# Optimization experiments

Measured on AMD Instinct MI355X. Metric: run time of the kernel, lower is better.

Reference implementation:

```python
import jax, jax.numpy as jnp
import numpy as np

B, NKV, NQ, D, H = 4, 2048, 1024, 1024, 16
HD = D // H


def setup_inputs() -> dict:
    key = jax.random.key(0)
    ks = jax.random.split(key, 9)
    s = 0.02
    return {
        "x": jax.random.normal(ks[0], (B, NKV, D), jnp.float32),
        "y": jax.random.normal(ks[1], (B, NQ, D), jnp.float32),
        "mask": jax.random.randint(ks[2], (B, NQ, NKV), 0, 2, jnp.int32),
        "W_kv": jax.random.normal(ks[3], (D, 2 * D), jnp.float32) * s,
        "b_kv": jnp.zeros((2 * D,), jnp.float32),
        "W_q": jax.random.normal(ks[4], (D, D), jnp.float32) * s,
        "b_q": jnp.zeros((D,), jnp.float32),
        "W_o": jax.random.normal(ks[5], (D, D), jnp.float32) * s,
        "b_o": jnp.zeros((D,), jnp.float32),
    }


def reference(x, y, mask, W_kv, b_kv, W_q, b_q, W_o, b_o):
    b, nkv, _ = x.shape
    nq = y.shape[1]
    kv = x @ W_kv + b_kv                                  # [B, NKV, 2D]
    q = y @ W_q + b_q                                     # [B, NQ, D]
    kv = kv.reshape(b, nkv, H, 2 * HD).transpose(0, 2, 1, 3)  # [B,H,NKV,2HD]
    q = q.reshape(b, nq, H, HD).transpose(0, 2, 1, 3)         # [B,H,NQ,HD]
    k, v = kv[..., :HD], kv[..., HD:]
    scores = jnp.einsum('bhqd,bhkd->bhqk', q, k) / jnp.sqrt(jnp.float32(HD))
    scores = jnp.where(mask[:, None, :, :] == 0, jnp.float32(-1e20), scores)
    attn = jax.nn.softmax(scores, axis=-1)
    vals = jnp.einsum('bhqk,bhkd->bhqd', attn, v)          # [B,H,NQ,HD]
    vals = vals.transpose(0, 2, 1, 3).reshape(b, nq, D)
    return vals @ W_o + b_o
```

## Files before the change

### kernel.cpp

```cpp
#include <hip/hip_runtime.h>
#include <hip/hip_bf16.h>
#include <math.h>

#define B_   4
#define NKV_ 2048
#define NQ_  1024
#define D_   1024
#define H_   16
#define HD_  64

typedef __attribute__((ext_vector_type(8))) short bf16x8;
typedef __attribute__((ext_vector_type(4))) float f32x4;

#define MFMA16x32(a, b, c) __builtin_amdgcn_mfma_f32_16x16x32_bf16((a), (b), (c), 0, 0, 0)

#define SC_LOG2 0.1803368801111244f

__device__ __forceinline__ short f2bf(float f) {
    unsigned u = __builtin_bit_cast(unsigned, f);
    u = (u + 0x7fff + ((u >> 16) & 1)) >> 16;
    return (short)u;
}
__device__ __forceinline__ unsigned cvt_pk_bf16(float lo, float hi) {
    unsigned r;
    asm("v_cvt_pk_bf16_f32 %0, %1, %2" : "=v"(r) : "v"(lo), "v"(hi));
    return r;
}
__device__ __forceinline__ void gload_lds16(const void* g, void* l) {
    __builtin_amdgcn_global_load_lds(
        (const __attribute__((address_space(1))) void*)g,
        (__attribute__((address_space(3))) void*)l, 16, 0, 0);
}
__device__ __forceinline__ void barrier_raw() {
    asm volatile("" ::: "memory");
    __builtin_amdgcn_s_barrier();
    asm volatile("" ::: "memory");
}

__global__ __launch_bounds__(256)
void prep(const float* __restrict__ Wkv, short* __restrict__ Tkv,
          const float* __restrict__ Wq,  short* __restrict__ Tq,
          const float* __restrict__ Wo,  short* __restrict__ To,
          const int* __restrict__ mask,  unsigned short* __restrict__ m16,
          const float* __restrict__ x,   short* __restrict__ xh, int n4x,
          const float* __restrict__ y,   short* __restrict__ yh, int n4y)
{
    const int bid = (int)blockIdx.x;
    if (bid < 4096) {
        const float* W; short* T; int K, N, bx, by;
        if (bid < 2048)      { W = Wkv; T = Tkv; K = D_; N = 2 * D_; bx = bid & 63;          by = bid >> 6; }
        else if (bid < 3072) { W = Wq;  T = Tq;  K = D_; N = D_;     bx = (bid - 2048) & 31; by = (bid - 2048) >> 5; }
        else                 { W = Wo;  T = To;  K = D_; N = D_;     bx = (bid - 3072) & 31; by = (bid - 3072) >> 5; }
        __shared__ float tile[32][33];
        const int tx = threadIdx.x & 31, ty = threadIdx.x >> 5;
        const int n0 = bx * 32, k0 = by * 32;
#pragma unroll
        for (int i = 0; i < 4; ++i)
            tile[ty + 8 * i][tx] = W[(size_t)(k0 + ty + 8 * i) * N + n0 + tx];
        __syncthreads();
#pragma unroll
        for (int i = 0; i < 4; ++i)
            T[(size_t)(n0 + ty + 8 * i) * K + k0 + tx] = f2bf(tile[tx][ty + 8 * i]);
    } else if (bid < 4608) {
        const int w = (bid - 4096) * 256 + threadIdx.x;
        const int4* pp = reinterpret_cast<const int4*>(mask + (size_t)w * 64);
        unsigned wg0 = 0, wg1 = 0, wg2 = 0, wg3 = 0;
#pragma unroll
        for (int i = 0; i < 16; ++i) {
            const int4 v = pp[i];
            const unsigned nib = (unsigned)(v.x != 0) | ((unsigned)(v.y != 0) << 1)
                               | ((unsigned)(v.z != 0) << 2) | ((unsigned)(v.w != 0) << 3);
            const unsigned sh = 4u * (unsigned)(i >> 2);
            if ((i & 3) == 0) wg0 |= nib << sh;
            else if ((i & 3) == 1) wg1 |= nib << sh;
            else if ((i & 3) == 2) wg2 |= nib << sh;
            else wg3 |= nib << sh;
        }
        ushort4 o;
        o.x = (unsigned short)wg0; o.y = (unsigned short)wg1;
        o.z = (unsigned short)wg2; o.w = (unsigned short)wg3;
        reinterpret_cast<ushort4*>(m16)[w] = o;
    } else {
        const int ntot = n4x + n4y;
        for (int i = (bid - 4608) * 256 + threadIdx.x; i < ntot; i += 2048 * 256) {
            const float4 v = (i < n4x)
                ? reinterpret_cast<const float4*>(x)[i]
                : reinterpret_cast<const float4*>(y)[i - n4x];
            short4 h;
            h.x = f2bf(v.x); h.y = f2bf(v.y); h.z = f2bf(v.z); h.w = f2bf(v.w);
            if (i < n4x) reinterpret_cast<short4*>(xh)[i] = h;
            else         reinterpret_cast<short4*>(yh)[i - n4x] = h;
        }
    }
}

__device__ __forceinline__
void gemm_body(int mode, int bidl,
               const short* __restrict__ Ahi, const short* __restrict__ Bhi,
               const float* __restrict__ bias, void* __restrict__ out0,
               void* __restrict__ out1, int M, int N, int K)
{
    __shared__ short At[3][4096];
    __shared__ short Bt[3][4096];

    const int t    = threadIdx.x;
    const int wave = t >> 6;
    const int lane = t & 63;
    const int fr   = lane & 15;
    const int kq   = lane >> 4;

    const int gx  = N >> 7;
    const int gy  = M >> 7;
    const int lgx = __builtin_ctz(gx);
    const int xcd = bidl & 7;
    const int j   = bidl >> 3;
    const int m0  = (xcd * (gy >> 3) + (j >> lgx)) * 128;
    const int n0  = (j & (gx - 1)) * 128;

    const int wm0 = (wave & 1) * 64;
    const int wn0 = (wave >> 1) * 64;
    const int NT  = K >> 5;

    const int r1 = t >> 2,         g1 = (t & 3) ^ ((r1 >> 1) & 3);
    const int r2 = (t + 256) >> 2, g2 = (t & 3) ^ ((r2 >> 1) & 3);

    f32x4 acc[4][4];
#pragma unroll
    for (int i = 0; i < 4; ++i)
#pragma unroll
        for (int j2 = 0; j2 < 4; ++j2) acc[i][j2] = f32x4{0.f, 0.f, 0.f, 0.f};

    auto stage = [&](int sb, int it) {
        const int kk = it << 5;
        gload_lds16(Ahi + (size_t)(m0 + r1) * K + kk + 8 * g1, &At[sb][wave * 512]);
        gload_lds16(Ahi + (size_t)(m0 + r2) * K + kk + 8 * g2, &At[sb][2048 + wave * 512]);
        gload_lds16(Bhi + (size_t)(n0 + r1) * K + kk + 8 * g1, &Bt[sb][wave * 512]);
        gload_lds16(Bhi + (size_t)(n0 + r2) * K + kk + 8 * g2, &Bt[sb][2048 + wave * 512]);
    };

    stage(0, 0);
    if (NT > 1) stage(1, 1);

    const int gsw = ((kq ^ ((fr >> 1) & 3)) << 3);
    for (int it = 0; it < NT; ++it) {
        if (it + 1 < NT) asm volatile("s_waitcnt vmcnt(4)" ::: "memory");
        else             asm volatile("s_waitcnt vmcnt(0)" ::: "memory");
        barrier_raw();

        const int cb = it % 3;
        bf16x8 af[4], bf[4];
#pragma unroll
        for (int i = 0; i < 4; ++i) {
            af[i] = *reinterpret_cast<const bf16x8*>(&At[cb][(wm0 + i * 16 + fr) * 32 + gsw]);
            bf[i] = *reinterpret_cast<const bf16x8*>(&Bt[cb][(wn0 + i * 16 + fr) * 32 + gsw]);
        }
        if (it + 2 < NT) stage((it + 2) % 3, it + 2);

        __builtin_amdgcn_s_setprio(1);
#pragma unroll
        for (int i = 0; i < 4; ++i)
#pragma unroll
            for (int j2 = 0; j2 < 4; ++j2)
                acc[i][j2] = MFMA16x32(af[i], bf[j2], acc[i][j2]);
        __builtin_amdgcn_s_setprio(0);
    }

#pragma unroll
    for (int i = 0; i < 4; ++i) {
#pragma unroll
        for (int j2 = 0; j2 < 4; ++j2) {
#pragma unroll
            for (int r = 0; r < 4; ++r) {
                const int m = m0 + wm0 + i * 16 + (lane >> 4) * 4 + r;
                const int n = n0 + wn0 + j2 * 16 + fr;
                const float v = acc[i][j2][r] + bias[n];
                if (mode == 0) {
                    short* K_ = (short*)out0;
                    short* Vt = (short*)out1;
                    const int b  = m >> 11;
                    const int nk = m & 2047;
                    const int h  = n >> 7;
                    const int c  = n & 127;
                    const int bh = b * H_ + h;
                    if (c < 64)
                        K_[(((size_t)bh * NKV_ + nk) << 6) + c] = f2bf(v);
                    else
                        Vt[((size_t)bh * 64 + (c - 64)) * NKV_ + nk] = f2bf(v);
                } else if (mode == 1) {
                    short* Q_ = (short*)out0;
                    const int b = m >> 10;
                    const int q = m & 1023;
                    const int h = n >> 6;
                    const int d = n & 63;
                    Q_[(((size_t)(b * H_ + h) * NQ_ + q) << 6) + d] =
                        f2bf(v * SC_LOG2);
                } else {
                    ((float*)out0)[(size_t)m * N + n] = v;
                }
            }
        }
    }
}

__global__ __launch_bounds__(256)
void proj(const short* __restrict__ xhi, const short* __restrict__ Wkvt,
          const float* __restrict__ b_kv, short* __restrict__ Kbf,
          short* __restrict__ Vtbf,
          const short* __restrict__ yhi, const short* __restrict__ Wqt,
          const float* __restrict__ b_q, short* __restrict__ Qbf)
{
    const int bid = (int)blockIdx.x;
    if (bid < 1024)
        gemm_body(0, bid, xhi, Wkvt, b_kv, Kbf, Vtbf, B_ * NKV_, 2 * D_, D_);
    else
        gemm_body(1, bid - 1024, yhi, Wqt, b_q, Qbf, nullptr, B_ * NQ_, D_, D_);
}

__global__ __launch_bounds__(256)
void ogemm(const short* __restrict__ Ahi, const short* __restrict__ Bhi,
           const float* __restrict__ bias, float* __restrict__ out)
{
    __shared__ short At[3][2048];
    __shared__ short Bt[3][4096];

    const int M = B_ * NQ_, N = D_, K = D_;
    const int t    = threadIdx.x;
    const int wave = t >> 6;
    const int lane = t & 63;
    const int fr   = lane & 15;
    const int kq   = lane >> 4;

    const int gx  = N >> 7;
    const int gy  = M >> 6;
    const int lgx = __builtin_ctz(gx);
    const int bid = (int)blockIdx.x;
    const int xcd = bid & 7;
    const int j   = bid >> 3;
    const int m0  = (xcd * (gy >> 3) + (j >> lgx)) * 64;
    const int n0  = (j & (gx - 1)) * 128;

    const int wm0 = (wave & 1) * 32;
    const int wn0 = (wave >> 1) * 64;
    const int NT  = K >> 5;

    const int rA = t >> 2, gA = (t & 3) ^ ((rA >> 1) & 3);
    const int r1 = t >> 2,         g1 = (t & 3) ^ ((r1 >> 1) & 3);
    const int r2 = (t + 256) >> 2, g2 = (t & 3) ^ ((r2 >> 1) & 3);

    f32x4 acc[2][4];
#pragma unroll
    for (int i = 0; i < 2; ++i)
#pragma unroll
        for (int j2 = 0; j2 < 4; ++j2) acc[i][j2] = f32x4{0.f, 0.f, 0.f, 0.f};

    auto stage = [&](int sb, int it) {
        const int kk = it << 5;
        gload_lds16(Ahi + (size_t)(m0 + rA) * K + kk + 8 * gA, &At[sb][wave * 512]);
        gload_lds16(Bhi + (size_t)(n0 + r1) * K + kk + 8 * g1, &Bt[sb][wave * 512]);
        gload_lds16(Bhi + (size_t)(n0 + r2) * K + kk + 8 * g2, &Bt[sb][2048 + wave * 512]);
    };

    stage(0, 0);
    if (NT > 1) stage(1, 1);

    const int gsw = ((kq ^ ((fr >> 1) & 3)) << 3);
    for (int it = 0; it < NT; ++it) {
        if (it + 1 < NT) asm volatile("s_waitcnt vmcnt(3)" ::: "memory");
        else             asm volatile("s_waitcnt vmcnt(0)" ::: "memory");
        barrier_raw();

        const int cb = it % 3;
        bf16x8 af[2], bf[4];
#pragma unroll
        for (int i = 0; i < 2; ++i)
            af[i] = *reinterpret_cast<const bf16x8*>(&At[cb][(wm0 + i * 16 + fr) * 32 + gsw]);
#pragma unroll
        for (int i = 0; i < 4; ++i)
            bf[i] = *reinterpret_cast<const bf16x8*>(&Bt[cb][(wn0 + i * 16 + fr) * 32 + gsw]);
        if (it + 2 < NT) stage((it + 2) % 3, it + 2);

        __builtin_amdgcn_s_setprio(1);
#pragma unroll
        for (int i = 0; i < 2; ++i)
#pragma unroll
            for (int j2 = 0; j2 < 4; ++j2)
                acc[i][j2] = MFMA16x32(af[i], bf[j2], acc[i][j2]);
        __builtin_amdgcn_s_setprio(0);
    }

#pragma unroll
    for (int i = 0; i < 2; ++i)
#pragma unroll
        for (int j2 = 0; j2 < 4; ++j2)
#pragma unroll
            for (int r = 0; r < 4; ++r) {
                const int m = m0 + wm0 + i * 16 + (lane >> 4) * 4 + r;
                const int n = n0 + wn0 + j2 * 16 + fr;
                out[(size_t)m * N + n] = acc[i][j2][r] + bias[n];
            }
}

__global__ __launch_bounds__(512)
void attn_mfma(const short* __restrict__ Q, const short* __restrict__ K,
               const short* __restrict__ Vt,
               const unsigned short* __restrict__ m16,
               float* __restrict__ Opart, float* __restrict__ Lpart)
{
    __shared__ short KtL[2][4096];
    __shared__ short VtL[2][4096];
    __shared__ short PsL[8192];

    const int t    = threadIdx.x;
    const int wave = t >> 6;
    const int lane = t & 63;
    const int fr   = lane & 15;
    const int g    = lane >> 4;

    const int bid  = (int)blockIdx.x;
    const int xcd  = bid & 7;
    const int j    = bid >> 3;
    const int bh   = xcd * 8 + (j >> 4);
    const int rest = j & 15;
    const int half = rest & 1;
    const int b    = bh >> 4;
    const int h    = bh & 15;
    const int wq0  = (rest >> 1) * 128 + wave * 16;

    const int kts = half * 16;
    const int kte = kts + 16;

    const short* Kg  = K  + (size_t)bh * NKV_ * 64;
    const short* Vtg = Vt + (size_t)bh * 64 * NKV_;

    bf16x8 qf0, qf1;
    {
        const short* Qg = Q + ((size_t)bh * NQ_ + wq0 + fr) * 64 + g * 8;
        qf0 = *reinterpret_cast<const bf16x8*>(Qg);
        qf1 = *reinterpret_cast<const bf16x8*>(Qg + 32);
    }

    bf16x8 ones;
#pragma unroll
    for (int i = 0; i < 8; ++i) ones[i] = (short)0x3F80;

    f32x4 acc_o[4];
#pragma unroll
    for (int n = 0; n < 4; ++n) acc_o[n] = f32x4{0.f, 0.f, 0.f, 0.f};
    f32x4 lacc = f32x4{0.f, 0.f, 0.f, 0.f};

    const unsigned short* mbp =
        m16 + ((size_t)b * NQ_ + wq0 + fr) * (NKV_ / 64) * 4 + g;

    const int r8   = lane >> 3;
    const int csw  = ((lane & 7) << 3) ^ (r8 << 3);
    const int swzf = (fr & 7) << 3;
    short* PsW = PsL + wave * (16 * 64);

    auto stage = [&](int nb, int kt0) {
        const short* sK = Kg + (size_t)(kt0 + wave * 8 + r8) * 64 + csw;
        gload_lds16(sK, &KtL[nb][(wave * 8) * 64]);
        const short* sV = Vtg + (size_t)(wave * 8 + r8) * NKV_ + kt0 + csw;
        gload_lds16(sV, &VtL[nb][(wave * 8) * 64]);
    };

    stage(0, kts * 64);
    asm volatile("s_waitcnt vmcnt(0)" ::: "memory");
    __syncthreads();

    const int kcol0 = (8 * g) ^ swzf;
    const int kcol1 = (32 + 8 * g) ^ swzf;

    int cur = 0;
    for (int kt = kts; kt < kte; ++kt) {
        if (kt + 1 < kte) stage(cur ^ 1, (kt + 1) * 64);

        const unsigned mskv = mbp[(size_t)kt * 4];

        const short* KB = &KtL[cur][fr * 64];
        f32x4 s_acc[4];
        __builtin_amdgcn_s_setprio(1);
#pragma unroll
        for (int t4 = 0; t4 < 4; ++t4) {
            s_acc[t4] = f32x4{0.f, 0.f, 0.f, 0.f};
            const bf16x8 kf0 = *reinterpret_cast<const bf16x8*>(KB + t4 * 1024 + kcol0);
            const bf16x8 kf1 = *reinterpret_cast<const bf16x8*>(KB + t4 * 1024 + kcol1);
            s_acc[t4] = MFMA16x32(kf0, qf0, s_acc[t4]);
            s_acc[t4] = MFMA16x32(kf1, qf1, s_acc[t4]);
        }
        __builtin_amdgcn_s_setprio(0);

        float p[16];
#pragma unroll
        for (int t4 = 0; t4 < 4; ++t4)
#pragma unroll
            for (int r = 0; r < 4; ++r) {
                const int i = 4 * t4 + r;
                const float e = __builtin_amdgcn_exp2f(s_acc[t4][r]);
                p[i] = ((mskv >> i) & 1u) ? e : 0.f;
            }

#pragma unroll
        for (int t4 = 0; t4 < 4; ++t4) {
            uint2 w;
            w.x = cvt_pk_bf16(p[4 * t4 + 0], p[4 * t4 + 1]);
            w.y = cvt_pk_bf16(p[4 * t4 + 2], p[4 * t4 + 3]);
            *reinterpret_cast<uint2*>(&PsW[fr * 64 + ((16 * t4 + 4 * g) ^ swzf)]) = w;
        }

        {
            const bf16x8 pf0 = *reinterpret_cast<const bf16x8*>(&PsW[fr * 64 + kcol0]);
            const bf16x8 pf1 = *reinterpret_cast<const bf16x8*>(&PsW[fr * 64 + kcol1]);
            const short* VB = &VtL[cur][fr * 64];
            __builtin_amdgcn_s_setprio(1);
            lacc = MFMA16x32(ones, pf0, lacc);
            lacc = MFMA16x32(ones, pf1, lacc);
#pragma unroll
            for (int n = 0; n < 4; ++n) {
                const bf16x8 vf0 = *reinterpret_cast<const bf16x8*>(VB + n * 1024 + kcol0);
                const bf16x8 vf1 = *reinterpret_cast<const bf16x8*>(VB + n * 1024 + kcol1);
                acc_o[n] = MFMA16x32(vf0, pf0, acc_o[n]);
                acc_o[n] = MFMA16x32(vf1, pf1, acc_o[n]);
            }
            __builtin_amdgcn_s_setprio(0);
        }

        asm volatile("s_waitcnt vmcnt(0)" ::: "memory");
        __syncthreads();
        cur ^= 1;
    }

    float* Op = Opart + (size_t)half * (B_ * NQ_ * D_);
    const size_t obase = ((size_t)b * NQ_ + wq0 + fr) * D_ + h * 64;
#pragma unroll
    for (int n = 0; n < 4; ++n) {
        float4 v;
        v.x = acc_o[n][0]; v.y = acc_o[n][1];
        v.z = acc_o[n][2]; v.w = acc_o[n][3];
        *reinterpret_cast<float4*>(&Op[obase + 16 * n + 4 * g]) = v;
    }
    if (g == 0)
        Lpart[(size_t)half * (B_ * H_ * NQ_) + (size_t)bh * NQ_ + wq0 + fr] = lacc[0];
}

__global__ __launch_bounds__(256)
void combine(const float* __restrict__ Opart, const float* __restrict__ Lpart,
             short* __restrict__ valshi)
{
    const size_t npart = (size_t)B_ * NQ_ * D_;
    const int n4 = (int)(npart / 4);
    for (int i = blockIdx.x * 256 + threadIdx.x; i < n4; i += 2048 * 256) {
        const int row  = i >> 8;
        const int h    = (i & 255) >> 4;
        const int b    = row >> 10;
        const int q    = row & 1023;
        const float4 o0 = reinterpret_cast<const float4*>(Opart)[i];
        const float4 o1 = reinterpret_cast<const float4*>(Opart + npart)[i];
        const size_t li = (size_t)(b * H_ + h) * NQ_ + q;
        const float inv = 1.f / (Lpart[li] + Lpart[(size_t)B_ * H_ * NQ_ + li]);
        short4 hh;
        hh.x = f2bf((o0.x + o1.x) * inv);
        hh.y = f2bf((o0.y + o1.y) * inv);
        hh.z = f2bf((o0.z + o1.z) * inv);
        hh.w = f2bf((o0.w + o1.w) * inv);
        reinterpret_cast<short4*>(valshi)[i] = hh;
    }
}

extern "C" void kernel_launch(void* const* d_in, const int* in_sizes, int n_in,
                              void* d_out, int out_size, void* d_ws, size_t ws_size,
                              hipStream_t stream)
{
    const float* x    = (const float*)d_in[0];
    const float* y    = (const float*)d_in[1];
    const int*   mask = (const int*)  d_in[2];
    const float* W_kv = (const float*)d_in[3];
    const float* b_kv = (const float*)d_in[4];
    const float* W_q  = (const float*)d_in[5];
    const float* b_q  = (const float*)d_in[6];
    const float* W_o  = (const float*)d_in[7];
    const float* b_o  = (const float*)d_in[8];
    float* out = (float*)d_out;

    char* p = (char*)d_ws;
    auto take = [&](size_t bytes) { char* r = p; p += bytes; return r; };
    short* xhi    = (short*)take((size_t)B_ * NKV_ * D_ * 2);
    short* yhi    = (short*)take((size_t)B_ * NQ_ * D_ * 2);
    short* Wkvthi = (short*)take((size_t)2 * D_ * D_ * 2);
    short* Wqthi  = (short*)take((size_t)D_ * D_ * 2);
    short* Wothi  = (short*)take((size_t)D_ * D_ * 2);
    short* Kbf    = (short*)take((size_t)B_ * H_ * NKV_ * HD_ * 2);
    short* Vtbf   = (short*)take((size_t)B_ * H_ * HD_ * NKV_ * 2);
    short* Qbf    = (short*)take((size_t)B_ * H_ * NQ_ * HD_ * 2);
    unsigned short* m16 =
        (unsigned short*)take((size_t)B_ * NQ_ * (NKV_ / 64) * 4 * 2);
    float* Opart  = (float*)take((size_t)2 * B_ * NQ_ * D_ * 4);
    float* Lpart  = (float*)take((size_t)2 * B_ * H_ * NQ_ * 4);
    short* valshi = xhi;

    prep<<<6656, 256, 0, stream>>>(W_kv, Wkvthi, W_q, Wqthi, W_o, Wothi,
                                   mask, m16,
                                   x, xhi, B_ * NKV_ * D_ / 4,
                                   y, yhi, B_ * NQ_ * D_ / 4);

    proj<<<1280, 256, 0, stream>>>(xhi, Wkvthi, b_kv, Kbf, Vtbf,
                                   yhi, Wqthi, b_q, Qbf);

    attn_mfma<<<1024, 512, 0, stream>>>(Qbf, Kbf, Vtbf, m16, Opart, Lpart);

    combine<<<2048, 256, 0, stream>>>(Opart, Lpart, valshi);

    ogemm<<<512, 256, 0, stream>>>(valshi, Wothi, b_o, out);

    (void)in_sizes; (void)n_in; (void)out_size; (void)ws_size;
}
```

Baseline: 182.4 us.

## Enlarge projection GEMM tiles to 256x256 with 512 threads and 4-stage pipeline

```diff
diff --git a/kernel.cpp b/kernel.cpp
--- a/kernel.cpp
+++ b/kernel.cpp
@@ -95,70 +95,78 @@
 }
 
 __device__ __forceinline__
-void gemm_body(int mode, int bidl,
-               const short* __restrict__ Ahi, const short* __restrict__ Bhi,
-               const float* __restrict__ bias, void* __restrict__ out0,
-               void* __restrict__ out1, int M, int N, int K)
-{
-    __shared__ short At[3][4096];
-    __shared__ short Bt[3][4096];
+void gemm256_body(int mode, int bidl,
+                  const short* __restrict__ A, const short* __restrict__ Bm,
+                  const float* __restrict__ bias, void* __restrict__ out0,
+                  void* __restrict__ out1, int M, int N)
+{
+    constexpr int K  = 1024;
+    constexpr int NT = K / 32;
+
+    __shared__ short At[4][8192];
+    __shared__ short Bt[4][8192];
 
     const int t    = threadIdx.x;
     const int wave = t >> 6;
     const int lane = t & 63;
     const int fr   = lane & 15;
     const int kq   = lane >> 4;
-
-    const int gx  = N >> 7;
-    const int gy  = M >> 7;
+    const int wm0  = (wave >> 2) * 128;
+    const int wn0  = (wave & 3) * 64;
+
+    const int gx  = N >> 8;
+    const int gy  = M >> 8;
     const int lgx = __builtin_ctz(gx);
     const int xcd = bidl & 7;
     const int j   = bidl >> 3;
-    const int m0  = (xcd * (gy >> 3) + (j >> lgx)) * 128;
-    const int n0  = (j & (gx - 1)) * 128;
-
-    const int wm0 = (wave & 1) * 64;
-    const int wn0 = (wave >> 1) * 64;
-    const int NT  = K >> 5;
-
-    const int r1 = t >> 2,         g1 = (t & 3) ^ ((r1 >> 1) & 3);
-    const int r2 = (t + 256) >> 2, g2 = (t & 3) ^ ((r2 >> 1) & 3);
-
-    f32x4 acc[4][4];
-#pragma unroll
-    for (int i = 0; i < 4; ++i)
+    const int m0  = (xcd * (gy >> 3) + (j >> lgx)) * 256;
+    const int n0  = (j & (gx - 1)) * 256;
+
+    const int r1 = t >> 2;
+    const int g1 = (t & 3) ^ ((r1 >> 1) & 3);
+    const int r2 = r1 + 128;
+
+    f32x4 acc[8][4];
+#pragma unroll
+    for (int i = 0; i < 8; ++i)
 #pragma unroll
         for (int j2 = 0; j2 < 4; ++j2) acc[i][j2] = f32x4{0.f, 0.f, 0.f, 0.f};
 
     auto stage = [&](int sb, int it) {
         const int kk = it << 5;
-        gload_lds16(Ahi + (size_t)(m0 + r1) * K + kk + 8 * g1, &At[sb][wave * 512]);
-        gload_lds16(Ahi + (size_t)(m0 + r2) * K + kk + 8 * g2, &At[sb][2048 + wave * 512]);
-        gload_lds16(Bhi + (size_t)(n0 + r1) * K + kk + 8 * g1, &Bt[sb][wave * 512]);
-        gload_lds16(Bhi + (size_t)(n0 + r2) * K + kk + 8 * g2, &Bt[sb][2048 + wave * 512]);
+        gload_lds16(A  + (size_t)(m0 + r1) * K + kk + 8 * g1, &At[sb][wave * 512]);
+        gload_lds16(A  + (size_t)(m0 + r2) * K + kk + 8 * g1, &At[sb][4096 + wave * 512]);
+        gload_lds16(Bm + (size_t)(n0 + r1) * K + kk + 8 * g1, &Bt[sb][wave * 512]);
+        gload_lds16(Bm + (size_t)(n0 + r2) * K + kk + 8 * g1, &Bt[sb][4096 + wave * 512]);
     };
 
     stage(0, 0);
-    if (NT > 1) stage(1, 1);
+    stage(1, 1);
+    stage(2, 2);
 
     const int gsw = ((kq ^ ((fr >> 1) & 3)) << 3);
     for (int it = 0; it < NT; ++it) {
-        if (it + 1 < NT) asm volatile("s_waitcnt vmcnt(4)" ::: "memory");
-        else             asm volatile("s_waitcnt vmcnt(0)" ::: "memory");
+        if (it < NT - 2)       asm volatile("s_waitcnt vmcnt(8)" ::: "memory");
+        else if (it == NT - 2) asm volatile("s_waitcnt vmcnt(4)" ::: "memory");
+        else                   asm volatile("s_waitcnt vmcnt(0)" ::: "memory");
         barrier_raw();
 
-        const int cb = it % 3;
-        bf16x8 af[4], bf[4];
-#pragma unroll
-        for (int i = 0; i < 4; ++i) {
-            af[i] = *reinterpret_cast<const bf16x8*>(&At[cb][(wm0 + i * 16 + fr) * 32 + gsw]);
-            bf[i] = *reinterpret_cast<const bf16x8*>(&Bt[cb][(wn0 + i * 16 + fr) * 32 + gsw]);
-        }
-        if (it + 2 < NT) stage((it + 2) % 3, it + 2);
+        const int cb = it & 3;
+        bf16x8 af[8], bf[4];
+#pragma unroll
+        for (int i = 0; i < 8; ++i)
+            af[i] = *reinterpret_cast<const bf16x8*>(
+                &At[cb][(wm0 + i * 16 + fr) * 32 + gsw]);
+#pragma unroll
+        for (int i = 0; i < 4; ++i)
+            bf[i] = *reinterpret_cast<const bf16x8*>(
+                &Bt[cb][(wn0 + i * 16 + fr) * 32 + gsw]);
+
+        if (it + 3 < NT) stage((it + 3) & 3, it + 3);
 
         __builtin_amdgcn_s_setprio(1);
 #pragma unroll
-        for (int i = 0; i < 4; ++i)
+        for (int i = 0; i < 8; ++i)
 #pragma unroll
             for (int j2 = 0; j2 < 4; ++j2)
                 acc[i][j2] = MFMA16x32(af[i], bf[j2], acc[i][j2]);
@@ -166,7 +174,7 @@
     }
 
 #pragma unroll
-    for (int i = 0; i < 4; ++i) {
+    for (int i = 0; i < 8; ++i) {
 #pragma unroll
         for (int j2 = 0; j2 < 4; ++j2) {
 #pragma unroll
@@ -202,18 +210,18 @@
     }
 }
 
-__global__ __launch_bounds__(256)
-void proj(const short* __restrict__ xhi, const short* __restrict__ Wkvt,
-          const float* __restrict__ b_kv, short* __restrict__ Kbf,
-          short* __restrict__ Vtbf,
-          const short* __restrict__ yhi, const short* __restrict__ Wqt,
-          const float* __restrict__ b_q, short* __restrict__ Qbf)
+__global__ __launch_bounds__(512, 2)
+void proj256(const short* __restrict__ xhi, const short* __restrict__ Wkvt,
+             const float* __restrict__ b_kv, short* __restrict__ Kbf,
+             short* __restrict__ Vtbf,
+             const short* __restrict__ yhi, const short* __restrict__ Wqt,
+             const float* __restrict__ b_q, short* __restrict__ Qbf)
 {
     const int bid = (int)blockIdx.x;
-    if (bid < 1024)
-        gemm_body(0, bid, xhi, Wkvt, b_kv, Kbf, Vtbf, B_ * NKV_, 2 * D_, D_);
+    if (bid < 256)
+        gemm256_body(0, bid, xhi, Wkvt, b_kv, Kbf, Vtbf, B_ * NKV_, 2 * D_);
     else
-        gemm_body(1, bid - 1024, yhi, Wqt, b_q, Qbf, nullptr, B_ * NQ_, D_, D_);
+        gemm256_body(1, bid - 256, yhi, Wqt, b_q, Qbf, nullptr, B_ * NQ_, D_);
 }
 
 __global__ __launch_bounds__(256)
@@ -502,8 +510,8 @@
                                    x, xhi, B_ * NKV_ * D_ / 4,
                                    y, yhi, B_ * NQ_ * D_ / 4);
 
-    proj<<<1280, 256, 0, stream>>>(xhi, Wkvthi, b_kv, Kbf, Vtbf,
-                                   yhi, Wqthi, b_q, Qbf);
+    proj256<<<320, 512, 0, stream>>>(xhi, Wkvthi, b_kv, Kbf, Vtbf,
+                                     yhi, Wqthi, b_q, Qbf);
 
     attn_mfma<<<1024, 512, 0, stream>>>(Qbf, Kbf, Vtbf, m16, Opart, Lpart);
 
```

After: 183.2 us. About the same (+0.5%).
